# Performance work log

Measured on AMD Instinct MI355X. Metric: run time of the kernel, lower is better.

Reference implementation:

```python
import jax, jax.numpy as jnp
import numpy as np

H = 96
NH = 4
HD = H // NH
SPARSITY = 0.5
LN_EPS = 1e-5


def _lstm_layer(xs, w_ih, w_hh, b_ih, b_hh):
    # xs: [B, T, I]; PyTorch gate order i, f, g, o
    B = xs.shape[0]
    Hd = w_hh.shape[1]
    def step(carry, x_t):
        h, c = carry
        gates = x_t @ w_ih.T + h @ w_hh.T + b_ih + b_hh  # [B, 4H]
        i, f, g, o = jnp.split(gates, 4, axis=-1)
        i = jax.nn.sigmoid(i); f = jax.nn.sigmoid(f)
        g = jnp.tanh(g); o = jax.nn.sigmoid(o)
        c = f * c + i * g
        h = o * jnp.tanh(c)
        return (h, c), h
    h0 = jnp.zeros((B, Hd), xs.dtype)
    c0 = jnp.zeros((B, Hd), xs.dtype)
    _, hs = jax.lax.scan(step, (h0, c0), xs.transpose(1, 0, 2))  # [T, B, H]
    return hs.transpose(1, 0, 2)


def _layer_norm(x, w, b):
    mu = jnp.mean(x, axis=-1, keepdims=True)
    var = jnp.mean((x - mu) ** 2, axis=-1, keepdims=True)
    return (x - mu) * jax.lax.rsqrt(var + LN_EPS) * w + b


def _split_heads(x, B, T):
    return x.reshape(B, T, NH, HD).transpose(0, 2, 1, 3)  # [B, H, T, d]


def _sparse_attention(x, qw, kw, vw, ow):
    B, T, _ = x.shape
    q = _split_heads(x @ qw.T, B, T)
    k = _split_heads(x @ kw.T, B, T)
    v = _split_heads(x @ vw.T, B, T)
    scores = jnp.einsum('bhtd,bhsd->bhts', q, k) / np.sqrt(HD).astype(np.float32)
    num_keep = int(T * SPARSITY)
    topv, _ = jax.lax.top_k(scores, num_keep)
    kth = topv[..., -1:]  # threshold == k-th largest (equiv to topk+scatter mask for distinct values)
    scores = jnp.where(scores >= kth, scores, -jnp.inf)
    attn = jax.nn.softmax(scores, axis=-1)  # dropout is identity in eval
    out = jnp.einsum('bhts,bhsd->bhtd', attn, v)
    out = out.transpose(0, 2, 1, 3).reshape(B, T, H)
    return out @ ow.T


def _mha(x, in_w, in_b, out_w, out_b):
    B, T, _ = x.shape
    qkv = x @ in_w.T + in_b  # [B, T, 3H]
    q, k, v = jnp.split(qkv, 3, axis=-1)
    q = _split_heads(q, B, T); k = _split_heads(k, B, T); v = _split_heads(v, B, T)
    scores = jnp.einsum('bhtd,bhsd->bhts', q, k) / np.sqrt(HD).astype(np.float32)
    attn = jax.nn.softmax(scores, axis=-1)
    out = jnp.einsum('bhts,bhsd->bhtd', attn, v)
    out = out.transpose(0, 2, 1, 3).reshape(B, T, H)
    return out @ out_w.T + out_b


def _encoder_layer(x, in_w, in_b, out_w, out_b, l1_w, l1_b, l2_w, l2_b, ln1_w, ln1_b, ln2_w, ln2_b):
    # PyTorch TransformerEncoderLayer, post-norm, ReLU, eval (no dropout)
    x = _layer_norm(x + _mha(x, in_w, in_b, out_w, out_b), ln1_w, ln1_b)
    ff = jax.nn.relu(x @ l1_w.T + l1_b) @ l2_w.T + l2_b
    return _layer_norm(x + ff, ln2_w, ln2_b)


def setup_inputs() -> dict:
    key = jax.random.key(0)
    ks = iter(jax.random.split(key, 40))
    B, T, I = 16, 1024, 64
    FF = 2 * H
    def rnd(shape, scale=0.05):
        return (jax.random.normal(next(ks), shape, dtype=jnp.float32) * scale)
    inp = {
        'x': jax.random.normal(next(ks), (B, T, I), dtype=jnp.float32),
        'w_ih0': rnd((4 * H, I)), 'w_hh0': rnd((4 * H, H)),
        'b_ih0': rnd((4 * H,)), 'b_hh0': rnd((4 * H,)),
        'w_ih1': rnd((4 * H, H)), 'w_hh1': rnd((4 * H, H)),
        'b_ih1': rnd((4 * H,)), 'b_hh1': rnd((4 * H,)),
        'qw': rnd((H, H)), 'kw': rnd((H, H)), 'vw': rnd((H, H)), 'ow': rnd((H, H)),
        'enc_in_w': rnd((2, 3 * H, H)), 'enc_in_b': rnd((2, 3 * H)),
        'enc_out_w': rnd((2, H, H)), 'enc_out_b': rnd((2, H)),
        'enc_l1_w': rnd((2, FF, H)), 'enc_l1_b': rnd((2, FF)),
        'enc_l2_w': rnd((2, H, FF)), 'enc_l2_b': rnd((2, H)),
        'enc_ln1_w': jnp.ones((2, H), jnp.float32), 'enc_ln1_b': jnp.zeros((2, H), jnp.float32),
        'enc_ln2_w': jnp.ones((2, H), jnp.float32), 'enc_ln2_b': jnp.zeros((2, H), jnp.float32),
        'fc_w': rnd((1, H)), 'fc_b': rnd((1,)),
    }
    return inp


def reference(x, w_ih0, w_hh0, b_ih0, b_hh0, w_ih1, w_hh1, b_ih1, b_hh1,
              qw, kw, vw, ow,
              enc_in_w, enc_in_b, enc_out_w, enc_out_b,
              enc_l1_w, enc_l1_b, enc_l2_w, enc_l2_b,
              enc_ln1_w, enc_ln1_b, enc_ln2_w, enc_ln2_b,
              fc_w, fc_b):
    h = _lstm_layer(x, w_ih0, w_hh0, b_ih0, b_hh0)
    h = _lstm_layer(h, w_ih1, w_hh1, b_ih1, b_hh1)
    h = _sparse_attention(h, qw, kw, vw, ow)
    for i in range(2):
        h = _encoder_layer(h, enc_in_w[i], enc_in_b[i], enc_out_w[i], enc_out_b[i],
                           enc_l1_w[i], enc_l1_b[i], enc_l2_w[i], enc_l2_b[i],
                           enc_ln1_w[i], enc_ln1_b[i], enc_ln2_w[i], enc_ln2_b[i])
    return h[:, -1, :] @ fc_w.T + fc_b  # [B, 1]
```

## Files before the change

### kernel.cpp

```cpp
#include <hip/hip_runtime.h>
#include <cstdint>
#include <cmath>

#define T_SEQ 1024
#define BATCH 16
#define HID 96
#define G4 384
#define QKV_LD 288
#define HDIM 24
#define KKEEP 512
#define SCALE 0.20412414523193154f
#define L2E 1.4426950408889634f

typedef _Float16 half2v __attribute__((ext_vector_type(2)));
typedef __bf16 bf16x8 __attribute__((ext_vector_type(8)));
typedef float  f32x4v __attribute__((ext_vector_type(4)));

__device__ __forceinline__ float wred_sum(float v){
#pragma unroll
  for (int o=32;o;o>>=1) v += __shfl_xor(v,o,64);
  return v;
}
__device__ __forceinline__ float wred_max(float v){
#pragma unroll
  for (int o=32;o;o>>=1) v = fmaxf(v,__shfl_xor(v,o,64));
  return v;
}
__device__ __forceinline__ unsigned fmono(float f){
  unsigned u = __float_as_uint(f);
  return (u & 0x80000000u) ? ~u : (u | 0x80000000u);
}
__device__ __forceinline__ float sigf(float x){
  return __builtin_amdgcn_rcpf(1.f + __builtin_amdgcn_exp2f(-L2E*x));
}
__device__ __forceinline__ float tanhf2(float x){
  return fmaf(-2.f, __builtin_amdgcn_rcpf(1.f + __builtin_amdgcn_exp2f((2.f*L2E)*x)), 1.f);
}
template<int CTRL>
__device__ __forceinline__ float dpp_add_f(float v){
  int s = __builtin_amdgcn_update_dpp(0, __float_as_int(v), CTRL, 0xF, 0xF, true);
  return v + __int_as_float(s);
}
__device__ __forceinline__ float dpp_red4(float v){
  v = dpp_add_f<0xB1>(v);
  v = dpp_add_f<0x4E>(v);
  return v;
}
#if __has_builtin(__builtin_amdgcn_fdot2)
__device__ __forceinline__ float fdot2(half2v a, half2v b, float c){
  return __builtin_amdgcn_fdot2(a, b, c, false);
}
#else
__device__ __forceinline__ float fdot2(half2v a, half2v b, float c){
  return fmaf((float)a[0], (float)b[0], fmaf((float)a[1], (float)b[1], c));
}
#endif
__device__ __forceinline__ half2v pkh2(float a, float b){
  return __builtin_bit_cast(half2v, __builtin_amdgcn_cvt_pkrtz(a, b));
}
__device__ __forceinline__ unsigned short f2bf(float f){
  unsigned u = __float_as_uint(f);
  return (unsigned short)((u + 0x7fffu + ((u>>16)&1u)) >> 16);
}
__device__ __forceinline__ f32x4v mfma16(uint4 a, uint4 b, f32x4v c){
  return __builtin_amdgcn_mfma_f32_16x16x32_bf16(
      __builtin_bit_cast(bf16x8, a), __builtin_bit_cast(bf16x8, b), c, 0, 0, 0);
}

template<int K>
__global__ __launch_bounds__(256)
void gemm_mfma(const float* __restrict__ A, const float* __restrict__ W,
               const float* __restrict__ b1, const float* __restrict__ b2,
               float* __restrict__ C, int N, int ldc, int coff, int relu)
{
  __shared__ unsigned short As[128][K+8];
  __shared__ unsigned short Ws[64][K+8];
  const int tid = threadIdx.x;
  const int wave = tid >> 6, lane = tid & 63;
  const int ln = lane & 15, kq = lane >> 4;
  const int m0 = blockIdx.y * 128, n0 = blockIdx.x * 64;

  for (int idx = tid; idx < 128*(K/4); idx += 256){
    const int row = idx / (K/4), c4 = idx - row*(K/4);
    const float4 v = *(const float4*)(A + (size_t)(m0+row)*K + c4*4);
    ushort4 s = {f2bf(v.x), f2bf(v.y), f2bf(v.z), f2bf(v.w)};
    *(ushort4*)&As[row][c4*4] = s;
  }
  for (int idx = tid; idx < 64*(K/4); idx += 256){
    const int row = idx / (K/4), c4 = idx - row*(K/4);
    float4 v = {0,0,0,0};
    const int gn = n0 + row;
    if (gn < N) v = *(const float4*)(W + (size_t)gn*K + c4*4);
    ushort4 s = {f2bf(v.x), f2bf(v.y), f2bf(v.z), f2bf(v.w)};
    *(ushort4*)&Ws[row][c4*4] = s;
  }
  __syncthreads();

  f32x4v acc[2][4];
#pragma unroll
  for (int mi=0;mi<2;++mi)
#pragma unroll
    for (int ni=0;ni<4;++ni){ f32x4v z = {0.f,0.f,0.f,0.f}; acc[mi][ni] = z; }

#pragma unroll
  for (int ks=0; ks<K/32; ++ks){
    uint4 af[2], bf[4];
#pragma unroll
    for (int mi=0;mi<2;++mi)
      af[mi] = *(const uint4*)&As[wave*32 + mi*16 + ln][ks*32 + kq*8];
#pragma unroll
    for (int ni=0;ni<4;++ni)
      bf[ni] = *(const uint4*)&Ws[ni*16 + ln][ks*32 + kq*8];
#pragma unroll
    for (int mi=0;mi<2;++mi)
#pragma unroll
      for (int ni=0;ni<4;++ni)
        acc[mi][ni] = mfma16(af[mi], bf[ni], acc[mi][ni]);
  }

#pragma unroll
  for (int ni=0;ni<4;++ni){
    const int gn = n0 + ni*16 + ln;
    if (gn >= N) continue;
    float bias = 0.f;
    if (b1) bias += b1[gn];
    if (b2) bias += b2[gn];
#pragma unroll
    for (int mi=0;mi<2;++mi){
      const int row = m0 + wave*32 + mi*16 + kq*4;
#pragma unroll
      for (int r=0;r<4;++r){
        float v = acc[mi][ni][r] + bias;
        if (relu) v = fmaxf(v, 0.f);
        C[(size_t)(row + r)*ldc + coff + gn] = v;
      }
    }
  }
}

__global__ __launch_bounds__(256)
void pack_qkv_kernel(const float* __restrict__ qw, const float* __restrict__ kw,
                     const float* __restrict__ vw, float* __restrict__ wqkv)
{
  const int i = blockIdx.x*256 + threadIdx.x;
  if (i < 9216)       wqkv[i] = qw[i];
  else if (i < 18432) wqkv[i] = kw[i-9216];
  else if (i < 27648) wqkv[i] = vw[i-18432];
}

__global__ __launch_bounds__(384)
void lstm_kernel(const float* __restrict__ pre, const float* __restrict__ w_hh,
                 float* __restrict__ hout)
{
  const int b = blockIdx.x;
  const int tid = threadIdx.x;
  const int q = tid & 3, j = tid >> 2;
  half2v w[4][12];
#pragma unroll
  for (int g=0; g<4; ++g){
    const float* wp = w_hh + (size_t)(g*96 + j)*96 + q*24;
#pragma unroll
    for (int k=0;k<12;++k){
      half2v t; t[0] = (_Float16)wp[2*k]; t[1] = (_Float16)wp[2*k+1];
      w[g][k] = t;
    }
  }
  __shared__ _Float16 h_lds[96];
  float c = 0.f;
  if (tid < 96) h_lds[tid] = (_Float16)0.f;
  __syncthreads();

  const float* prow = pre + (size_t)b*T_SEQ*G4 + q*96 + j;
  float* hrow = hout + (size_t)b*T_SEQ*HID;
  float pf[4];
#pragma unroll
  for (int i=0;i<4;++i) pf[i] = prow[(size_t)i*G4];

  for (int tb=0; tb<T_SEQ; tb+=4){
#pragma unroll
    for (int u=0; u<4; ++u){
      const int t = tb + u;
      const float pcur = pf[u];
      int tn = t + 4; if (tn > T_SEQ-1) tn = T_SEQ-1;
      pf[u] = prow[(size_t)tn*G4];
      const uint4 a0 = *(const uint4*)(h_lds + q*24);
      const uint4 a1 = *(const uint4*)(h_lds + q*24 + 8);
      const uint4 a2 = *(const uint4*)(h_lds + q*24 + 16);
      half2v h2[12];
      h2[0]=__builtin_bit_cast(half2v, a0.x); h2[1]=__builtin_bit_cast(half2v, a0.y);
      h2[2]=__builtin_bit_cast(half2v, a0.z); h2[3]=__builtin_bit_cast(half2v, a0.w);
      h2[4]=__builtin_bit_cast(half2v, a1.x); h2[5]=__builtin_bit_cast(half2v, a1.y);
      h2[6]=__builtin_bit_cast(half2v, a1.z); h2[7]=__builtin_bit_cast(half2v, a1.w);
      h2[8]=__builtin_bit_cast(half2v, a2.x); h2[9]=__builtin_bit_cast(half2v, a2.y);
      h2[10]=__builtin_bit_cast(half2v, a2.z); h2[11]=__builtin_bit_cast(half2v, a2.w);

      float sA0=0.f,sA1=0.f,sA2=0.f,sA3=0.f;
      float sB0=0.f,sB1=0.f,sB2=0.f,sB3=0.f;
#pragma unroll
      for (int k=0;k<12;k+=2){
        sA0 = fdot2(w[0][k], h2[k], sA0);  sB0 = fdot2(w[0][k+1], h2[k+1], sB0);
        sA1 = fdot2(w[1][k], h2[k], sA1);  sB1 = fdot2(w[1][k+1], h2[k+1], sB1);
        sA2 = fdot2(w[2][k], h2[k], sA2);  sB2 = fdot2(w[2][k+1], h2[k+1], sB2);
        sA3 = fdot2(w[3][k], h2[k], sA3);  sB3 = fdot2(w[3][k+1], h2[k+1], sB3);
      }
      float s0 = sA0+sB0, s1 = sA1+sB1, s2 = sA2+sB2, s3 = sA3+sB3;
      s0 += (q==0) ? pcur : 0.f;
      s1 += (q==1) ? pcur : 0.f;
      s2 += (q==2) ? pcur : 0.f;
      s3 += (q==3) ? pcur : 0.f;
      s0 = dpp_red4(s0);
      s1 = dpp_red4(s1);
      s2 = dpp_red4(s2);
      s3 = dpp_red4(s3);
      const float iv = sigf(s0), fv = sigf(s1);
      const float gv = tanhf2(s2), ov = sigf(s3);
      c = fmaf(fv, c, iv*gv);
      const float hv = ov * tanhf2(c);
      if (q == 0){
        h_lds[j] = (_Float16)hv;
        hrow[t*HID + j] = hv;
      }
      __syncthreads();
    }
  }
}

__global__ __launch_bounds__(512, 1)
void attn_kernel(const float* __restrict__ qkv, float* __restrict__ out, int sparse)
{
  __shared__ float kl[24][260];
  unsigned* klh = (unsigned*)&kl[0][0];
  const int tid = threadIdx.x;
  const int wave = tid >> 6, lane = tid & 63;
  const int bh = blockIdx.x >> 6;
  const int b = bh >> 2, h = bh & 3;
  const int tq = ((blockIdx.x & 63) << 4) + wave*2;
  const size_t base = (size_t)b * T_SEQ;
  const int hoff = h * HDIM;
  half2v q20[12], q21[12];
  {
    const float* qp0 = qkv + (base + tq)*QKV_LD + hoff;
    const float* qp1 = qp0 + QKV_LD;
#pragma unroll
    for (int d4=0; d4<6; ++d4){
      float4 t0 = *(const float4*)(qp0 + d4*4);
      float4 t1 = *(const float4*)(qp1 + d4*4);
      q20[d4*2+0] = pkh2(t0.x, t0.y); q20[d4*2+1] = pkh2(t0.z, t0.w);
      q21[d4*2+0] = pkh2(t1.x, t1.y); q21[d4*2+1] = pkh2(t1.z, t1.w);
    }
  }
  float sc0[16], sc1[16];
  for (int c=0;c<4;++c){
    __syncthreads();
#pragma unroll
    for (int rep=0;rep<3;++rep){
      int p = rep*512 + tid;
      int sl = p/6, d4 = p - sl*6;
      const float4 kv = *(const float4*)(qkv + (base + (c<<8) + sl)*QKV_LD + 96 + hoff + d4*4);
      klh[(d4*2+0)*260 + sl] = __builtin_bit_cast(unsigned, pkh2(kv.x, kv.y));
      klh[(d4*2+1)*260 + sl] = __builtin_bit_cast(unsigned, pkh2(kv.z, kv.w));
    }
    __syncthreads();
    float a0=0.f,a1=0.f,a2=0.f,a3=0.f;
    float b0=0.f,b1v=0.f,b2v=0.f,b3=0.f;
#pragma unroll
    for (int dp=0; dp<12; ++dp){
      const uint4 kd = *(const uint4*)&klh[dp*260 + lane*4];
      const half2v k0 = __builtin_bit_cast(half2v, kd.x);
      const half2v k1 = __builtin_bit_cast(half2v, kd.y);
      const half2v k2 = __builtin_bit_cast(half2v, kd.z);
      const half2v k3 = __builtin_bit_cast(half2v, kd.w);
      a0 = fdot2(q20[dp], k0, a0); a1 = fdot2(q20[dp], k1, a1);
      a2 = fdot2(q20[dp], k2, a2); a3 = fdot2(q20[dp], k3, a3);
      b0 = fdot2(q21[dp], k0, b0); b1v = fdot2(q21[dp], k1, b1v);
      b2v = fdot2(q21[dp], k2, b2v); b3 = fdot2(q21[dp], k3, b3);
    }
    sc0[c*4+0]=a0*SCALE; sc0[c*4+1]=a1*SCALE; sc0[c*4+2]=a2*SCALE; sc0[c*4+3]=a3*SCALE;
    sc1[c*4+0]=b0*SCALE; sc1[c*4+1]=b1v*SCALE; sc1[c*4+2]=b2v*SCALE; sc1[c*4+3]=b3*SCALE;
  }
  float inv0, inv1;
#define SOFTMAX_ROW(SC, INV)                                                  \
  {                                                                           \
    float m_loc = SC[0];                                                      \
    _Pragma("unroll")                                                         \
    for (int i=1;i<16;++i) m_loc = fmaxf(m_loc, SC[i]);                       \
    const float m = wred_max(m_loc);                                          \
    float sum_loc = 0.f;                                                      \
    if (sparse){                                                              \
      unsigned u[16];                                                         \
      _Pragma("unroll")                                                       \
      for (int i=0;i<16;++i) u[i] = fmono(SC[i]);                             \
      unsigned prefix = 0;                                                    \
      for (int bit=31; bit>=0; --bit){                                        \
        const unsigned test = prefix | (1u<<bit);                             \
        int cnt = 0;                                                          \
        _Pragma("unroll")                                                     \
        for (int i=0;i<16;++i)                                                \
          cnt += (int)__popcll(__ballot(u[i] >= test));                       \
        if (cnt >= KKEEP) prefix = test;                                      \
      }                                                                       \
      _Pragma("unroll")                                                       \
      for (int i=0;i<16;++i){                                                 \
        float e = (u[i] >= prefix) ? __expf(SC[i]-m) : 0.f;                   \
        SC[i] = e; sum_loc += e;                                              \
      }                                                                       \
    } else {                                                                  \
      _Pragma("unroll")                                                       \
      for (int i=0;i<16;++i){                                                 \
        float e = __expf(SC[i]-m);                                            \
        SC[i] = e; sum_loc += e;                                              \
      }                                                                       \
    }                                                                         \
    INV = 1.f / wred_sum(sum_loc);                                            \
  }
  SOFTMAX_ROW(sc0, inv0)
  SOFTMAX_ROW(sc1, inv1)
#undef SOFTMAX_ROW
#pragma unroll
  for (int i=0;i<16;++i){ sc0[i] *= inv0; sc1[i] *= inv1; }
  float acc0[24] = {}, acc1[24] = {};
  for (int c=0;c<4;++c){
    __syncthreads();
#pragma unroll
    for (int rep=0;rep<3;++rep){
      int p = rep*512 + tid;
      int sl = p/6, d4 = p - sl*6;
      const float4 vv = *(const float4*)(qkv + (base + (c<<8) + sl)*QKV_LD + 192 + hoff + d4*4);
      kl[d4*4+0][sl]=vv.x; kl[d4*4+1][sl]=vv.y; kl[d4*4+2][sl]=vv.z; kl[d4*4+3][sl]=vv.w;
    }
    __syncthreads();
    const float w00=sc0[c*4], w01=sc0[c*4+1], w02=sc0[c*4+2], w03=sc0[c*4+3];
    const float w10=sc1[c*4], w11=sc1[c*4+1], w12=sc1[c*4+2], w13=sc1[c*4+3];
#pragma unroll
    for (int d=0; d<24; ++d){
      const float4 vd = *(const float4*)&kl[d][lane*4];
      acc0[d] += w00*vd.x + w01*vd.y + w02*vd.z + w03*vd.w;
      acc1[d] += w10*vd.x + w11*vd.y + w12*vd.z + w13*vd.w;
    }
  }
#pragma unroll
  for (int d=0; d<24; ++d){ acc0[d] = wred_sum(acc0[d]); acc1[d] = wred_sum(acc1[d]); }
  if (lane == 0){
    float* op0 = out + (base + tq)*HID + hoff;
    float* op1 = op0 + HID;
#pragma unroll
    for (int d4=0; d4<6; ++d4){
      float4 t0 = {acc0[d4*4], acc0[d4*4+1], acc0[d4*4+2], acc0[d4*4+3]};
      float4 t1 = {acc1[d4*4], acc1[d4*4+1], acc1[d4*4+2], acc1[d4*4+3]};
      *(float4*)(op0 + d4*4) = t0;
      *(float4*)(op1 + d4*4) = t1;
    }
  }
}

__global__ __launch_bounds__(64)
void attn_last_kernel(const float* __restrict__ qkv, float* __restrict__ out)
{
  const int bh = blockIdx.x, b = bh>>2, h = bh&3;
  const int lane = threadIdx.x;
  const size_t base = (size_t)b*T_SEQ;
  const int hoff = h*HDIM;
  float q[24];
  {
    const float* qp = qkv + (base + T_SEQ-1)*QKV_LD + hoff;
#pragma unroll
    for (int d4=0; d4<6; ++d4){
      float4 t = *(const float4*)(qp + d4*4);
      q[d4*4]=t.x; q[d4*4+1]=t.y; q[d4*4+2]=t.z; q[d4*4+3]=t.w;
    }
  }
  float sc[16];
#pragma unroll 4
  for (int i=0;i<16;++i){
    const float* kp = qkv + (base + i*64 + lane)*QKV_LD + 96 + hoff;
    float a = 0.f;
#pragma unroll
    for (int d4=0; d4<6; ++d4){
      float4 kv = *(const float4*)(kp + d4*4);
      a += q[d4*4]*kv.x + q[d4*4+1]*kv.y + q[d4*4+2]*kv.z + q[d4*4+3]*kv.w;
    }
    sc[i] = a*SCALE;
  }
  float m_loc = sc[0];
#pragma unroll
  for (int i=1;i<16;++i) m_loc = fmaxf(m_loc, sc[i]);
  const float m = wred_max(m_loc);
  float sum_loc = 0.f;
#pragma unroll
  for (int i=0;i<16;++i){ sc[i] = __expf(sc[i]-m); sum_loc += sc[i]; }
  const float inv = 1.f / wred_sum(sum_loc);
  float acc[24] = {};
#pragma unroll 4
  for (int i=0;i<16;++i){
    const float* vp = qkv + (base + i*64 + lane)*QKV_LD + 192 + hoff;
    const float wgt = sc[i]*inv;
#pragma unroll
    for (int d4=0; d4<6; ++d4){
      float4 vv = *(const float4*)(vp + d4*4);
      acc[d4*4]   += wgt*vv.x; acc[d4*4+1] += wgt*vv.y;
      acc[d4*4+2] += wgt*vv.z; acc[d4*4+3] += wgt*vv.w;
    }
  }
#pragma unroll
  for (int d=0; d<24; ++d) acc[d] = wred_sum(acc[d]);
  if (lane == 0){
    float* op = out + (base + T_SEQ-1)*HID + hoff;
#pragma unroll
    for (int d4=0; d4<6; ++d4){
      float4 t = {acc[d4*4], acc[d4*4+1], acc[d4*4+2], acc[d4*4+3]};
      *(float4*)(op + d4*4) = t;
    }
  }
}

__global__ __launch_bounds__(256)
void resln_kernel(const float* __restrict__ x, const float* __restrict__ y,
                  const float* __restrict__ w, const float* __restrict__ bb,
                  float* __restrict__ out)
{
  const int row = blockIdx.x*4 + (threadIdx.x>>6);
  const int lane = threadIdx.x & 63;
  const float* xr = x + (size_t)row*HID;
  const float* yr = y + (size_t)row*HID;
  float v0 = xr[lane] + yr[lane];
  float v1 = (lane < 32) ? (xr[64+lane] + yr[64+lane]) : 0.f;
  float mu = wred_sum(v0+v1) * (1.f/96.f);
  float d0 = v0-mu, d1 = (lane<32) ? (v1-mu) : 0.f;
  float var = wred_sum(d0*d0 + d1*d1) * (1.f/96.f);
  float rs = rsqrtf(var + 1e-5f);
  float* orow = out + (size_t)row*HID;
  orow[lane] = d0*rs*w[lane] + bb[lane];
  if (lane < 32) orow[64+lane] = d1*rs*w[64+lane] + bb[64+lane];
}

__device__ __forceinline__ float block_sum_192(float v, float* red){
  v = wred_sum(v);
  const int tid = threadIdx.x;
  if ((tid & 63) == 0) red[tid>>6] = v;
  __syncthreads();
  float r = red[0]+red[1]+red[2];
  __syncthreads();
  return r;
}

__global__ __launch_bounds__(192)
void tail_kernel(const float* __restrict__ xin, const float* __restrict__ mha,
                 const float* __restrict__ out_w, const float* __restrict__ out_b,
                 const float* __restrict__ l1_w, const float* __restrict__ l1_b,
                 const float* __restrict__ l2_w, const float* __restrict__ l2_b,
                 const float* __restrict__ ln1w, const float* __restrict__ ln1b,
                 const float* __restrict__ ln2w, const float* __restrict__ ln2b,
                 const float* __restrict__ fcw, const float* __restrict__ fcb,
                 float* __restrict__ outp)
{
  const int b = blockIdx.x, tid = threadIdx.x;
  __shared__ float y[96], f1[192], mrow[96], red[3];
  const size_t row = ((size_t)b*T_SEQ + T_SEQ-1)*HID;
  if (tid < 96) mrow[tid] = mha[row + tid];
  __syncthreads();
  float r = 0.f;
  if (tid < 96){
    float p = out_b[tid];
    const float* wr = out_w + tid*96;
#pragma unroll 4
    for (int d=0; d<96; ++d) p += mrow[d]*wr[d];
    r = xin[row + tid] + p;
  }
  float mu = block_sum_192(tid<96 ? r : 0.f, red) * (1.f/96.f);
  float dv = tid<96 ? r-mu : 0.f;
  float var = block_sum_192(dv*dv, red) * (1.f/96.f);
  float rs = rsqrtf(var + 1e-5f);
  if (tid < 96) y[tid] = dv*rs*ln1w[tid] + ln1b[tid];
  __syncthreads();
  {
    float a = l1_b[tid];
    const float* wr = l1_w + tid*96;
#pragma unroll 4
    for (int d=0; d<96; ++d) a += y[d]*wr[d];
    f1[tid] = fmaxf(a, 0.f);
  }
  __syncthreads();
  float r2 = 0.f;
  if (tid < 96){
    float a = l2_b[tid];
    const float* wr = l2_w + tid*192;
#pragma unroll 4
    for (int d=0; d<192; ++d) a += f1[d]*wr[d];
    r2 = y[tid] + a;
  }
  float mu2 = block_sum_192(tid<96 ? r2 : 0.f, red) * (1.f/96.f);
  float dv2 = tid<96 ? r2-mu2 : 0.f;
  float var2 = block_sum_192(dv2*dv2, red) * (1.f/96.f);
  float rs2 = rsqrtf(var2 + 1e-5f);
  float z = tid<96 ? (dv2*rs2*ln2w[tid] + ln2b[tid]) : 0.f;
  float tot = block_sum_192(tid<96 ? z*fcw[tid] : 0.f, red);
  if (tid == 0) outp[b] = tot + fcb[0];
}

extern "C" void kernel_launch(void* const* d_in, const int* in_sizes, int n_in,
                              void* d_out, int out_size, void* d_ws, size_t ws_size,
                              hipStream_t stream)
{
  const float* x     = (const float*)d_in[0];
  const float* w_ih0 = (const float*)d_in[1];
  const float* w_hh0 = (const float*)d_in[2];
  const float* b_ih0 = (const float*)d_in[3];
  const float* b_hh0 = (const float*)d_in[4];
  const float* w_ih1 = (const float*)d_in[5];
  const float* w_hh1 = (const float*)d_in[6];
  const float* b_ih1 = (const float*)d_in[7];
  const float* b_hh1 = (const float*)d_in[8];
  const float* qw = (const float*)d_in[9];
  const float* kw = (const float*)d_in[10];
  const float* vw = (const float*)d_in[11];
  const float* ow = (const float*)d_in[12];
  const float* enc_in_w  = (const float*)d_in[13];
  const float* enc_in_b  = (const float*)d_in[14];
  const float* enc_out_w = (const float*)d_in[15];
  const float* enc_out_b = (const float*)d_in[16];
  const float* enc_l1_w  = (const float*)d_in[17];
  const float* enc_l1_b  = (const float*)d_in[18];
  const float* enc_l2_w  = (const float*)d_in[19];
  const float* enc_l2_b  = (const float*)d_in[20];
  const float* enc_ln1_w = (const float*)d_in[21];
  const float* enc_ln1_b = (const float*)d_in[22];
  const float* enc_ln2_w = (const float*)d_in[23];
  const float* enc_ln2_b = (const float*)d_in[24];
  const float* fc_w = (const float*)d_in[25];
  const float* fc_b = (const float*)d_in[26];
  float* outp = (float*)d_out;

  float* ws = (float*)d_ws;
  const size_t MT = (size_t)BATCH*T_SEQ;
  float* pre  = ws;
  float* bufA = pre  + MT*G4;
  float* bufB = bufA + MT*HID;
  float* bufC = bufB + MT*HID;
  float* wqkv = bufC + MT*HID;

  auto gemm = [&](const float* A, const float* W, const float* bb1, const float* bb2,
                  float* C, int N, int K, int ldc, int coff, int relu){
    dim3 grid((N+63)/64, 128);
    if (K == 64)
      gemm_mfma<64><<<grid, dim3(256), 0, stream>>>(A, W, bb1, bb2, C, N, ldc, coff, relu);
    else if (K == 96)
      gemm_mfma<96><<<grid, dim3(256), 0, stream>>>(A, W, bb1, bb2, C, N, ldc, coff, relu);
    else
      gemm_mfma<192><<<grid, dim3(256), 0, stream>>>(A, W, bb1, bb2, C, N, ldc, coff, relu);
  };

  pack_qkv_kernel<<<dim3(108), dim3(256), 0, stream>>>(qw, kw, vw, wqkv);

  gemm(x, w_ih0, b_ih0, b_hh0, pre, 384, 64, 384, 0, 0);
  lstm_kernel<<<dim3(BATCH), dim3(384), 0, stream>>>(pre, w_hh0, bufA);
  gemm(bufA, w_ih1, b_ih1, b_hh1, pre, 384, 96, 384, 0, 0);
  lstm_kernel<<<dim3(BATCH), dim3(384), 0, stream>>>(pre, w_hh1, bufB);
  gemm(bufB, wqkv, nullptr, nullptr, pre, 288, 96, QKV_LD, 0, 0);
  attn_kernel<<<dim3(4096), dim3(512), 0, stream>>>(pre, bufA, 1);
  gemm(bufA, ow, nullptr, nullptr, bufB, 96, 96, 96, 0, 0);
  gemm(bufB, enc_in_w, enc_in_b, nullptr, pre, 288, 96, QKV_LD, 0, 0);
  attn_kernel<<<dim3(4096), dim3(512), 0, stream>>>(pre, bufA, 0);
  gemm(bufA, enc_out_w, enc_out_b, nullptr, bufC, 96, 96, 96, 0, 0);
  resln_kernel<<<dim3(4096), dim3(256), 0, stream>>>(bufB, bufC, enc_ln1_w, enc_ln1_b, bufB);
  gemm(bufB, enc_l1_w, enc_l1_b, nullptr, pre, 192, 96, 192, 0, 1);
  gemm(pre, enc_l2_w, enc_l2_b, nullptr, bufC, 96, 192, 96, 0, 0);
  resln_kernel<<<dim3(4096), dim3(256), 0, stream>>>(bufB, bufC, enc_ln2_w, enc_ln2_b, bufB);
  gemm(bufB, enc_in_w + 288*96, enc_in_b + 288, nullptr, pre, 288, 96, QKV_LD, 0, 0);
  attn_last_kernel<<<dim3(64), dim3(64), 0, stream>>>(pre, bufA);
  tail_kernel<<<dim3(BATCH), dim3(192), 0, stream>>>(
      bufB, bufA,
      enc_out_w + 96*96, enc_out_b + 96,
      enc_l1_w + 192*96, enc_l1_b + 192,
      enc_l2_w + 96*192, enc_l2_b + 96,
      enc_ln1_w + 96, enc_ln1_b + 96,
      enc_ln2_w + 96, enc_ln2_b + 96,
      fc_w, fc_b, outp);
}
```

Before: 1.840 ms.

## Pipeline both LSTM layers concurrently with flag-based producer-consumer handoff

```diff
diff --git a/kernel.cpp b/kernel.cpp
--- a/kernel.cpp
+++ b/kernel.cpp
@@ -148,80 +148,197 @@
   else if (i < 27648) wqkv[i] = vw[i-18432];
 }
 
-__global__ __launch_bounds__(384)
-void lstm_kernel(const float* __restrict__ pre, const float* __restrict__ w_hh,
-                 float* __restrict__ hout)
-{
-  const int b = blockIdx.x;
+__global__ __launch_bounds__(384, 1)
+void lstm_pipe_kernel(const float* __restrict__ pre,
+                      const float* __restrict__ w_hh0,
+                      const float* __restrict__ w_ih1,
+                      const float* __restrict__ w_hh1,
+                      const float* __restrict__ b_ih1,
+                      const float* __restrict__ b_hh1,
+                      float* h0x, int* flag,
+                      float* __restrict__ hout)
+{
+  const int role = blockIdx.x >> 4, b = blockIdx.x & 15;
   const int tid = threadIdx.x;
   const int q = tid & 3, j = tid >> 2;
-  half2v w[4][12];
-#pragma unroll
-  for (int g=0; g<4; ++g){
-    const float* wp = w_hh + (size_t)(g*96 + j)*96 + q*24;
-#pragma unroll
-    for (int k=0;k<12;++k){
-      half2v t; t[0] = (_Float16)wp[2*k]; t[1] = (_Float16)wp[2*k+1];
-      w[g][k] = t;
-    }
-  }
   __shared__ _Float16 h_lds[96];
   float c = 0.f;
   if (tid < 96) h_lds[tid] = (_Float16)0.f;
-  __syncthreads();
-
-  const float* prow = pre + (size_t)b*T_SEQ*G4 + q*96 + j;
-  float* hrow = hout + (size_t)b*T_SEQ*HID;
-  float pf[4];
-#pragma unroll
-  for (int i=0;i<4;++i) pf[i] = prow[(size_t)i*G4];
-
-  for (int tb=0; tb<T_SEQ; tb+=4){
-#pragma unroll
-    for (int u=0; u<4; ++u){
-      const int t = tb + u;
-      const float pcur = pf[u];
-      int tn = t + 4; if (tn > T_SEQ-1) tn = T_SEQ-1;
-      pf[u] = prow[(size_t)tn*G4];
-      const uint4 a0 = *(const uint4*)(h_lds + q*24);
-      const uint4 a1 = *(const uint4*)(h_lds + q*24 + 8);
-      const uint4 a2 = *(const uint4*)(h_lds + q*24 + 16);
-      half2v h2[12];
-      h2[0]=__builtin_bit_cast(half2v, a0.x); h2[1]=__builtin_bit_cast(half2v, a0.y);
-      h2[2]=__builtin_bit_cast(half2v, a0.z); h2[3]=__builtin_bit_cast(half2v, a0.w);
-      h2[4]=__builtin_bit_cast(half2v, a1.x); h2[5]=__builtin_bit_cast(half2v, a1.y);
-      h2[6]=__builtin_bit_cast(half2v, a1.z); h2[7]=__builtin_bit_cast(half2v, a1.w);
-      h2[8]=__builtin_bit_cast(half2v, a2.x); h2[9]=__builtin_bit_cast(half2v, a2.y);
-      h2[10]=__builtin_bit_cast(half2v, a2.z); h2[11]=__builtin_bit_cast(half2v, a2.w);
-
-      float sA0=0.f,sA1=0.f,sA2=0.f,sA3=0.f;
-      float sB0=0.f,sB1=0.f,sB2=0.f,sB3=0.f;
-#pragma unroll
-      for (int k=0;k<12;k+=2){
-        sA0 = fdot2(w[0][k], h2[k], sA0);  sB0 = fdot2(w[0][k+1], h2[k+1], sB0);
-        sA1 = fdot2(w[1][k], h2[k], sA1);  sB1 = fdot2(w[1][k+1], h2[k+1], sB1);
-        sA2 = fdot2(w[2][k], h2[k], sA2);  sB2 = fdot2(w[2][k+1], h2[k+1], sB2);
-        sA3 = fdot2(w[3][k], h2[k], sA3);  sB3 = fdot2(w[3][k+1], h2[k+1], sB3);
+  const size_t h0base = (size_t)b * T_SEQ * HID;
+
+  if (role == 0){
+    half2v w[4][12];
+#pragma unroll
+    for (int g=0; g<4; ++g){
+      const float* wp = w_hh0 + (size_t)(g*96 + j)*96 + q*24;
+#pragma unroll
+      for (int k=0;k<12;++k){
+        half2v t; t[0] = (_Float16)wp[2*k]; t[1] = (_Float16)wp[2*k+1];
+        w[g][k] = t;
       }
-      float s0 = sA0+sB0, s1 = sA1+sB1, s2 = sA2+sB2, s3 = sA3+sB3;
-      s0 += (q==0) ? pcur : 0.f;
-      s1 += (q==1) ? pcur : 0.f;
-      s2 += (q==2) ? pcur : 0.f;
-      s3 += (q==3) ? pcur : 0.f;
-      s0 = dpp_red4(s0);
-      s1 = dpp_red4(s1);
-      s2 = dpp_red4(s2);
-      s3 = dpp_red4(s3);
-      const float iv = sigf(s0), fv = sigf(s1);
-      const float gv = tanhf2(s2), ov = sigf(s3);
-      c = fmaf(fv, c, iv*gv);
-      const float hv = ov * tanhf2(c);
-      if (q == 0){
-        h_lds[j] = (_Float16)hv;
-        hrow[t*HID + j] = hv;
+    }
+    __syncthreads();
+    const float* prow = pre + (size_t)b*T_SEQ*G4 + q*96 + j;
+    float pf[4];
+#pragma unroll
+    for (int i=0;i<4;++i) pf[i] = prow[(size_t)i*G4];
+    float hv_prev = 0.f;
+
+    for (int tb=0; tb<T_SEQ; tb+=4){
+#pragma unroll
+      for (int u=0; u<4; ++u){
+        const int t = tb + u;
+        if (q == 0 && t > 0)
+          __hip_atomic_store(&h0x[h0base + (size_t)(t-1)*HID + j], hv_prev,
+                             __ATOMIC_RELAXED, __HIP_MEMORY_SCOPE_AGENT);
+        if (tid == 0 && t > 0 && (t & 7) == 0)
+          __hip_atomic_store(&flag[b], t-1, __ATOMIC_RELEASE, __HIP_MEMORY_SCOPE_AGENT);
+        const float pcur = pf[u];
+        int tn = t + 4; if (tn > T_SEQ-1) tn = T_SEQ-1;
+        pf[u] = prow[(size_t)tn*G4];
+        const uint4 a0 = *(const uint4*)(h_lds + q*24);
+        const uint4 a1 = *(const uint4*)(h_lds + q*24 + 8);
+        const uint4 a2 = *(const uint4*)(h_lds + q*24 + 16);
+        half2v h2[12];
+        h2[0]=__builtin_bit_cast(half2v, a0.x); h2[1]=__builtin_bit_cast(half2v, a0.y);
+        h2[2]=__builtin_bit_cast(half2v, a0.z); h2[3]=__builtin_bit_cast(half2v, a0.w);
+        h2[4]=__builtin_bit_cast(half2v, a1.x); h2[5]=__builtin_bit_cast(half2v, a1.y);
+        h2[6]=__builtin_bit_cast(half2v, a1.z); h2[7]=__builtin_bit_cast(half2v, a1.w);
+        h2[8]=__builtin_bit_cast(half2v, a2.x); h2[9]=__builtin_bit_cast(half2v, a2.y);
+        h2[10]=__builtin_bit_cast(half2v, a2.z); h2[11]=__builtin_bit_cast(half2v, a2.w);
+        float sA0=0.f,sA1=0.f,sA2=0.f,sA3=0.f;
+        float sB0=0.f,sB1=0.f,sB2=0.f,sB3=0.f;
+#pragma unroll
+        for (int k=0;k<12;k+=2){
+          sA0 = fdot2(w[0][k], h2[k], sA0);  sB0 = fdot2(w[0][k+1], h2[k+1], sB0);
+          sA1 = fdot2(w[1][k], h2[k], sA1);  sB1 = fdot2(w[1][k+1], h2[k+1], sB1);
+          sA2 = fdot2(w[2][k], h2[k], sA2);  sB2 = fdot2(w[2][k+1], h2[k+1], sB2);
+          sA3 = fdot2(w[3][k], h2[k], sA3);  sB3 = fdot2(w[3][k+1], h2[k+1], sB3);
+        }
+        float s0 = sA0+sB0, s1 = sA1+sB1, s2 = sA2+sB2, s3 = sA3+sB3;
+        s0 += (q==0) ? pcur : 0.f;
+        s1 += (q==1) ? pcur : 0.f;
+        s2 += (q==2) ? pcur : 0.f;
+        s3 += (q==3) ? pcur : 0.f;
+        s0 = dpp_red4(s0); s1 = dpp_red4(s1);
+        s2 = dpp_red4(s2); s3 = dpp_red4(s3);
+        const float iv = sigf(s0), fv = sigf(s1);
+        const float gv = tanhf2(s2), ov = sigf(s3);
+        c = fmaf(fv, c, iv*gv);
+        const float hv = ov * tanhf2(c);
+        if (q == 0){
+          h_lds[j] = (_Float16)hv;
+          hv_prev = hv;
+        }
+        __syncthreads();
       }
-      __syncthreads();
-    }
+    }
+    if (q == 0)
+      __hip_atomic_store(&h0x[h0base + (size_t)(T_SEQ-1)*HID + j], hv_prev,
+                         __ATOMIC_RELAXED, __HIP_MEMORY_SCOPE_AGENT);
+    __syncthreads();
+    if (tid == 0)
+      __hip_atomic_store(&flag[b], T_SEQ, __ATOMIC_RELEASE, __HIP_MEMORY_SCOPE_AGENT);
+  } else {
+    half2v wih[4][12], whh[4][12];
+#pragma unroll
+    for (int g=0; g<4; ++g){
+      const float* wp1 = w_ih1 + (size_t)(g*96 + j)*96 + q*24;
+      const float* wp2 = w_hh1 + (size_t)(g*96 + j)*96 + q*24;
+#pragma unroll
+      for (int k=0;k<12;++k){
+        half2v t1; t1[0] = (_Float16)wp1[2*k]; t1[1] = (_Float16)wp1[2*k+1];
+        half2v t2; t2[0] = (_Float16)wp2[2*k]; t2[1] = (_Float16)wp2[2*k+1];
+        wih[g][k] = t1; whh[g][k] = t2;
+      }
+    }
+    const float biasq = b_ih1[q*96 + j] + b_hh1[q*96 + j];
+    float* hrow = hout + (size_t)b*T_SEQ*HID;
+    __syncthreads();
+
+#define L1_GATE(NEED)                                                          \
+    {                                                                          \
+      if (tid == 0){                                                           \
+        int f = __hip_atomic_load(&flag[b], __ATOMIC_ACQUIRE,                  \
+                                  __HIP_MEMORY_SCOPE_AGENT);                   \
+        while (f < (NEED)){                                                    \
+          __builtin_amdgcn_s_sleep(8);                                         \
+          f = __hip_atomic_load(&flag[b], __ATOMIC_ACQUIRE,                    \
+                                __HIP_MEMORY_SCOPE_AGENT);                     \
+        }                                                                      \
+      }                                                                        \
+      __syncthreads();                                                         \
+    }
+
+    float pfA[24], pfB[24];
+    L1_GATE(6)
+#pragma unroll
+    for (int k=0;k<24;++k){
+      pfA[k] = __hip_atomic_load(&h0x[h0base + 0*HID + q*24 + k],
+                                 __ATOMIC_RELAXED, __HIP_MEMORY_SCOPE_AGENT);
+      pfB[k] = __hip_atomic_load(&h0x[h0base + 1*HID + q*24 + k],
+                                 __ATOMIC_RELAXED, __HIP_MEMORY_SCOPE_AGENT);
+    }
+
+#define L1_STEP(T, PF)                                                         \
+    {                                                                          \
+      half2v g2[12];                                                           \
+      _Pragma("unroll")                                                        \
+      for (int k=0;k<12;++k) g2[k] = pkh2(PF[2*k], PF[2*k+1]);                 \
+      int tp = (T) + 2; if (tp > T_SEQ-1) tp = T_SEQ-1;                        \
+      _Pragma("unroll")                                                        \
+      for (int k=0;k<24;++k)                                                   \
+        PF[k] = __hip_atomic_load(&h0x[h0base + (size_t)tp*HID + q*24 + k],    \
+                                  __ATOMIC_RELAXED, __HIP_MEMORY_SCOPE_AGENT); \
+      const uint4 a0 = *(const uint4*)(h_lds + q*24);                          \
+      const uint4 a1 = *(const uint4*)(h_lds + q*24 + 8);                      \
+      const uint4 a2 = *(const uint4*)(h_lds + q*24 + 16);                     \
+      half2v h2[12];                                                           \
+      h2[0]=__builtin_bit_cast(half2v, a0.x); h2[1]=__builtin_bit_cast(half2v, a0.y); \
+      h2[2]=__builtin_bit_cast(half2v, a0.z); h2[3]=__builtin_bit_cast(half2v, a0.w); \
+      h2[4]=__builtin_bit_cast(half2v, a1.x); h2[5]=__builtin_bit_cast(half2v, a1.y); \
+      h2[6]=__builtin_bit_cast(half2v, a1.z); h2[7]=__builtin_bit_cast(half2v, a1.w); \
+      h2[8]=__builtin_bit_cast(half2v, a2.x); h2[9]=__builtin_bit_cast(half2v, a2.y); \
+      h2[10]=__builtin_bit_cast(half2v, a2.z); h2[11]=__builtin_bit_cast(half2v, a2.w); \
+      float sA0=0.f,sA1=0.f,sA2=0.f,sA3=0.f;                                   \
+      float sB0=0.f,sB1=0.f,sB2=0.f,sB3=0.f;                                   \
+      _Pragma("unroll")                                                        \
+      for (int k=0;k<12;++k){                                                  \
+        sA0 = fdot2(wih[0][k], g2[k], sA0);  sB0 = fdot2(whh[0][k], h2[k], sB0); \
+        sA1 = fdot2(wih[1][k], g2[k], sA1);  sB1 = fdot2(whh[1][k], h2[k], sB1); \
+        sA2 = fdot2(wih[2][k], g2[k], sA2);  sB2 = fdot2(whh[2][k], h2[k], sB2); \
+        sA3 = fdot2(wih[3][k], g2[k], sA3);  sB3 = fdot2(whh[3][k], h2[k], sB3); \
+      }                                                                        \
+      float s0 = sA0+sB0, s1 = sA1+sB1, s2 = sA2+sB2, s3 = sA3+sB3;            \
+      s0 += (q==0) ? biasq : 0.f;                                              \
+      s1 += (q==1) ? biasq : 0.f;                                              \
+      s2 += (q==2) ? biasq : 0.f;                                              \
+      s3 += (q==3) ? biasq : 0.f;                                              \
+      s0 = dpp_red4(s0); s1 = dpp_red4(s1);                                    \
+      s2 = dpp_red4(s2); s3 = dpp_red4(s3);                                    \
+      const float iv = sigf(s0), fv = sigf(s1);                                \
+      const float gv = tanhf2(s2), ov = sigf(s3);                              \
+      c = fmaf(fv, c, iv*gv);                                                  \
+      const float hv = ov * tanhf2(c);                                         \
+      if (q == 0){                                                             \
+        h_lds[j] = (_Float16)hv;                                               \
+        hrow[(size_t)(T)*HID + j] = hv;                                        \
+      }                                                                        \
+      __syncthreads();                                                         \
+    }
+
+    for (int tb=0; tb<T_SEQ; tb+=4){
+      if (tb > 0){
+        const int need = (tb+6 < T_SEQ) ? tb+6 : T_SEQ;
+        L1_GATE(need)
+      }
+      L1_STEP(tb+0, pfA)
+      L1_STEP(tb+1, pfB)
+      L1_STEP(tb+2, pfA)
+      L1_STEP(tb+3, pfB)
+    }
+#undef L1_STEP
+#undef L1_GATE
   }
 }
 
@@ -537,6 +654,7 @@
   float* bufB = bufA + MT*HID;
   float* bufC = bufB + MT*HID;
   float* wqkv = bufC + MT*HID;
+  int*   flag = (int*)(wqkv + 27648);
 
   auto gemm = [&](const float* A, const float* W, const float* bb1, const float* bb2,
                   float* C, int N, int K, int ldc, int coff, int relu){
@@ -549,12 +667,12 @@
       gemm_mfma<192><<<grid, dim3(256), 0, stream>>>(A, W, bb1, bb2, C, N, ldc, coff, relu);
   };
 
+  hipMemsetAsync(flag, 0, 16*sizeof(int), stream);
   pack_qkv_kernel<<<dim3(108), dim3(256), 0, stream>>>(qw, kw, vw, wqkv);
 
   gemm(x, w_ih0, b_ih0, b_hh0, pre, 384, 64, 384, 0, 0);
-  lstm_kernel<<<dim3(BATCH), dim3(384), 0, stream>>>(pre, w_hh0, bufA);
-  gemm(bufA, w_ih1, b_ih1, b_hh1, pre, 384, 96, 384, 0, 0);
-  lstm_kernel<<<dim3(BATCH), dim3(384), 0, stream>>>(pre, w_hh1, bufB);
+  lstm_pipe_kernel<<<dim3(32), dim3(384), 0, stream>>>(
+      pre, w_hh0, w_ih1, w_hh1, b_ih1, b_hh1, bufA, flag, bufB);
   gemm(bufB, wqkv, nullptr, nullptr, pre, 288, 96, QKV_LD, 0, 0);
   attn_kernel<<<dim3(4096), dim3(512), 0, stream>>>(pre, bufA, 1);
   gemm(bufA, ow, nullptr, nullptr, bufB, 96, 96, 96, 0, 0);
```

Result: slower. 2.112 ms (+14.8%).
